# Kernel optimization log

Measured on AMD Instinct MI355X. Metric: run time of the kernel, lower is better.

The kernel has to match this reference:

```python
import jax, jax.numpy as jnp
import numpy as np

B, N, P, K, C = 8, 4096, 4096, 32, 128  # batch, points, npoint, neighbors, channels (=mlp[-1])
W_OUT = 16  # weightnet output channels (from Linear(16*mlp[-1], mlp[-1]))
EPS = 1e-5


def setup_inputs() -> dict:
    key = jax.random.key(0)
    ks = jax.random.split(key, 9)
    xyz = jax.random.normal(ks[0], (B, P, 3), jnp.float32)
    points = jax.random.normal(ks[1], (B, N, C), jnp.float32)
    local_coordinates = jax.random.normal(ks[2], (B, P, K, 3), jnp.float32)
    neighbor_lists = jax.random.randint(ks[3], (B, P, K), 0, N)
    data_idx = jax.random.randint(ks[4], (B,), 0, B)
    Ww = jax.random.normal(ks[5], (3, W_OUT), jnp.float32) * 0.1   # weightnet (pointwise linear 3->16)
    bw = jnp.zeros((W_OUT,), jnp.float32)
    Wl = jax.random.normal(ks[6], (W_OUT * C, C), jnp.float32) * 0.02  # nn.Linear(16*mlp[-1], mlp[-1])
    bl = jnp.zeros((C,), jnp.float32)
    gamma = jnp.ones((C,), jnp.float32)   # BatchNorm1d weight
    beta = jnp.zeros((C,), jnp.float32)   # BatchNorm1d bias
    return {"xyz": xyz, "points": points, "local_coordinates": local_coordinates,
            "neighbor_lists": neighbor_lists, "data_idx": data_idx,
            "Ww": Ww, "bw": bw, "Wl": Wl, "bl": bl, "gamma": gamma, "beta": beta}


def reference(xyz, points, local_coordinates, neighbor_lists, data_idx, Ww, bw, Wl, bl, gamma, beta):
    b, p, k, _ = local_coordinates.shape
    c = points.shape[-1]
    # weightnet: pointwise map of 3-D local coordinates to 16 weight channels -> [B,P,K,16]
    weights = local_coordinates @ Ww + bw
    # irregular neighbor gather: data[b,p,k,:] = points[b, neighbor_lists[b,p,k], :] -> [B,P,K,C]
    data = points[jnp.arange(b)[:, None, None], neighbor_lists]
    # per-point weighted aggregation over K neighbors: [B,P,C,16] -> flatten to [B,P,C*16]
    new_points = jnp.einsum('bpkc,bpkw->bpcw', data, weights).reshape(b, p, c * weights.shape[-1])
    # batch reindex via data_idx
    new_points = new_points[data_idx]
    # linear tail: [B,P,C]
    new_points = new_points @ Wl + bl
    # BatchNorm1d over channel dim (training-mode batch stats), then ReLU: [B,C,P]
    x = new_points.transpose(0, 2, 1)
    mean = x.mean(axis=(0, 2), keepdims=True)
    var = x.var(axis=(0, 2), keepdims=True)
    x = (x - mean) * jax.lax.rsqrt(var + EPS) * gamma[None, :, None] + beta[None, :, None]
    return xyz, jax.nn.relu(x)
```

## Files before the change

### kernel.cpp

```cpp
#include <hip/hip_runtime.h>

#define Bn 8
#define Nn 4096
#define Pn 4096
#define Kn 32
#define Cn 128

using float4v = __attribute__((ext_vector_type(4))) float;
using short8  = __attribute__((ext_vector_type(8))) short;

__device__ __forceinline__ unsigned short bf16b(float f) {
  union { float f; unsigned u; } v; v.f = f;
  unsigned r = v.u + 0x7FFFu + ((v.u >> 16) & 1u);
  return (unsigned short)(r >> 16);
}

__device__ __forceinline__ unsigned pkhi(float x, float y) {
  return __builtin_amdgcn_perm(__float_as_uint(y), __float_as_uint(x), 0x07060302u);
}

__global__ __launch_bounds__(256) void prep(const float* __restrict__ Wl,
                                            unsigned short* __restrict__ WlT,
                                            const float* __restrict__ xyz,
                                            float* __restrict__ out,
                                            float* __restrict__ gacc) {
  __shared__ unsigned short tile[128 * 33];
  const int t = threadIdx.x, blk = blockIdx.x;
  if (blk < 64) {
#pragma unroll
    for (int i = 0; i < 16; ++i) {
      int idx = i * 256 + t;
      int kl = idx >> 7, n = idx & 127;
      tile[n * 33 + kl] = bf16b(Wl[(size_t)(blk * 32 + kl) * 128 + n]);
    }
    __syncthreads();
#pragma unroll
    for (int i = 0; i < 16; ++i) {
      int idx = i * 256 + t;
      int n = idx >> 5, kl = idx & 31;
      WlT[(size_t)n * 2048 + blk * 32 + kl] = tile[n * 33 + kl];
    }
  } else {
    if (blk == 64) gacc[t] = 0.f;
    const int i0 = (blk - 64) * 3072 + t * 12;
#pragma unroll
    for (int i = 0; i < 3; ++i)
      *(float4v*)(out + i0 + i * 4) = *(const float4v*)(xyz + i0 + i * 4);
  }
}

__global__ __launch_bounds__(256, 4) void fused(
    const float* __restrict__ points, const float* __restrict__ lc,
    const int* __restrict__ nl, const int* __restrict__ didx,
    const float* __restrict__ Ww, const float* __restrict__ bwv,
    const unsigned short* __restrict__ WlT, const float* __restrict__ blv,
    float* __restrict__ xout, float* __restrict__ gacc) {
  __shared__ float slab[4][2][512];
  __shared__ unsigned short Mlds[32 * 256];
  __shared__ int nlds[32 * 32];
  __shared__ float red[256];

  const int t = threadIdx.x, lane = t & 63, w = t >> 6;
  const int l15 = lane & 15, q = lane >> 4;
  const int b = blockIdx.x & 7;
  const int pg = blockIdx.x >> 3;
  const int p0 = pg * 32;
  const int db = didx[b];
  const char* __restrict__ pbase = (const char*)(points + (size_t)db * Nn * Cn);

  {
    int4 nv = *(const int4*)(nl + (size_t)(db * Pn + p0) * Kn + t * 4);
    nv.x <<= 9; nv.y <<= 9; nv.z <<= 9; nv.w <<= 9;
    *(int4*)&nlds[t * 4] = nv;
  }

  const float Ww0 = Ww[l15], Ww1 = Ww[16 + l15], Ww2 = Ww[32 + l15];
  const float bw0 = bwv[l15];

  short8 af[8];
#pragma unroll
  for (int i = 0; i < 8; ++i) {
    const int p = p0 + w * 8 + i;
    const int pk = (db * Pn + p) * Kn;
    const float* __restrict__ lcp = lc + (size_t)(pk + q * 8) * 3;
    float la[24];
#pragma unroll
    for (int v = 0; v < 6; ++v) *(float4v*)&la[v * 4] = *(const float4v*)(lcp + v * 4);
#pragma unroll
    for (int j = 0; j < 8; ++j) {
      float ww = bw0 + la[3 * j] * Ww0 + la[3 * j + 1] * Ww1 + la[3 * j + 2] * Ww2;
      af[i][j] = (short)bf16b(ww);
    }
  }

  float4v acc[2][2];
#pragma unroll
  for (int pt = 0; pt < 2; ++pt)
#pragma unroll
    for (int nt = 0; nt < 2; ++nt) acc[pt][nt] = (float4v){0.f, 0.f, 0.f, 0.f};

  __syncthreads();

  const unsigned short* __restrict__ bpt =
      WlT + (size_t)(w * 32 + l15) * 2048 + q * 8;
  const unsigned cvoff = (unsigned)(l15 * 4);

#define WAITV8 asm volatile("s_waitcnt vmcnt(8)" ::: "memory")
#define WAITV0 asm volatile("s_waitcnt vmcnt(0)" ::: "memory")

#define DMA(i, ct, bsel)                                                   \
  {                                                                        \
    const int pi_ = w * 8 + (i);                                           \
    int nk_[8];                                                            \
    *(int4*)&nk_[0] = *(const int4*)&nlds[pi_ * 32 + q * 8];               \
    *(int4*)&nk_[4] = *(const int4*)&nlds[pi_ * 32 + q * 8 + 4];           \
    _Pragma("unroll") for (int j = 0; j < 8; ++j)                          \
        __builtin_amdgcn_global_load_lds(                                  \
            (const __attribute__((address_space(1))) unsigned int*)        \
                (pbase + ((unsigned)nk_[j] + cvoff + (unsigned)((ct) * 64))), \
            (__attribute__((address_space(3))) unsigned int*)              \
                (&slab[w][bsel][(j) * 64]),                                \
            4, 0, 0);                                                      \
  }

#define FIN(i, fsrc)                                                       \
  {                                                                        \
    const int pi_ = w * 8 + (i);                                           \
    union { short8 s; unsigned u[4]; } bv_;                                \
    bv_.u[0] = pkhi(fsrc[0], fsrc[1]);                                     \
    bv_.u[1] = pkhi(fsrc[2], fsrc[3]);                                     \
    bv_.u[2] = pkhi(fsrc[4], fsrc[5]);                                     \
    bv_.u[3] = pkhi(fsrc[6], fsrc[7]);                                     \
    float4v d_ = {0.f, 0.f, 0.f, 0.f};                                     \
    d_ = __builtin_amdgcn_mfma_f32_16x16x32_bf16(af[i], bv_.s, d_, 0, 0, 0); \
    const unsigned off_ = (unsigned)(pi_ * 512 + ((l15 * 32 + q * 8) ^     \
        ((((pi_ & 7) ^ (l15 & 7)) & 7) << 4)));                            \
    uint2 u_;                                                              \
    u_.x = pkhi(d_[0], d_[1]);                                             \
    u_.y = pkhi(d_[2], d_[3]);                                             \
    *(uint2*)((char*)Mlds + off_) = u_;                                    \
  }

  for (int ct = 0; ct < 8; ++ct) {
    DMA(0, ct, 0)
    DMA(1, ct, 1)
#pragma unroll
    for (int i = 0; i < 8; ++i) {
      if (i < 7) { WAITV8; } else { WAITV0; }
      __builtin_amdgcn_sched_barrier(0);
      float f[8];
      const float* ls = &slab[w][i & 1][(unsigned)(q * 16 + l15)];
#pragma unroll
      for (int j = 0; j < 8; ++j) f[j] = ls[j * 64];
      FIN(i, f)
      if (i < 6) {
        __builtin_amdgcn_sched_barrier(0);
        DMA(i + 2, ct, i & 1)
      }
    }
    __syncthreads();
    const unsigned short* __restrict__ bp = bpt + ct * 256;
    short8 b0A = *(const short8*)(bp);
    short8 b1A = *(const short8*)(bp + 32768);
    __builtin_amdgcn_s_setprio(1);
#pragma unroll
    for (int ks = 0; ks < 8; ++ks) {
      short8 b0B, b1B;
      if (ks < 7) {
        b0B = *(const short8*)(bp + (ks + 1) * 32);
        b1B = *(const short8*)(bp + 32768 + (ks + 1) * 32);
      }
      const unsigned ax = (unsigned)((ks * 64 + q * 16) ^
          ((((l15 & 7) ^ ((ks * 2 + (q >> 1)) & 7)) & 7) << 4));
      short8 a0 = *(const short8*)((const char*)Mlds + l15 * 512 + ax);
      short8 a1 = *(const short8*)((const char*)Mlds + (16 + l15) * 512 + ax);
      acc[0][0] = __builtin_amdgcn_mfma_f32_16x16x32_bf16(a0, b0A, acc[0][0], 0, 0, 0);
      acc[0][1] = __builtin_amdgcn_mfma_f32_16x16x32_bf16(a0, b1A, acc[0][1], 0, 0, 0);
      acc[1][0] = __builtin_amdgcn_mfma_f32_16x16x32_bf16(a1, b0A, acc[1][0], 0, 0, 0);
      acc[1][1] = __builtin_amdgcn_mfma_f32_16x16x32_bf16(a1, b1A, acc[1][1], 0, 0, 0);
      b0A = b0B; b1A = b1B;
    }
    __builtin_amdgcn_s_setprio(0);
    __syncthreads();
  }
#undef DMA
#undef FIN
#undef WAITV8
#undef WAITV0

#pragma unroll
  for (int nt = 0; nt < 2; ++nt) {
    const int ch = w * 32 + nt * 16 + l15;
    const float bb = blv[ch];
    float s = 0.f, sq = 0.f;
#pragma unroll
    for (int pt = 0; pt < 2; ++pt) {
      float4v o;
#pragma unroll
      for (int r = 0; r < 4; ++r) {
        float v = acc[pt][nt][r] + bb; o[r] = v; s += v; sq += v * v;
      }
      *(float4v*)(xout + ((size_t)(b * Cn + ch)) * Pn + p0 + pt * 16 + q * 4) = o;
    }
    s += __shfl_xor(s, 16); s += __shfl_xor(s, 32);
    sq += __shfl_xor(sq, 16); sq += __shfl_xor(sq, 32);
    if (lane < 16) { red[ch] = s; red[128 + ch] = sq; }
  }
  __syncthreads();
  atomicAdd(&gacc[t], red[t]);
}

__global__ __launch_bounds__(256) void finalize_ln(float* __restrict__ x,
                                                   const float* __restrict__ gacc,
                                                   const float* __restrict__ gamma,
                                                   const float* __restrict__ beta) {
  const int idx = blockIdx.x * 256 + threadIdx.x;
  const int fi = idx * 4;
  const int c = (fi >> 12) & 127;
  const float inv = 1.f / 32768.f;
  const float mean = gacc[c] * inv;
  const float var = gacc[128 + c] * inv - mean * mean;
  const float scale = rsqrtf(var + 1e-5f) * gamma[c];
  const float shift = beta[c] - mean * scale;
  float4v v = *(float4v*)(x + fi);
#pragma unroll
  for (int r = 0; r < 4; ++r) v[r] = fmaxf(v[r] * scale + shift, 0.f);
  *(float4v*)(x + fi) = v;
}

extern "C" void kernel_launch(void* const* d_in, const int* in_sizes, int n_in,
                              void* d_out, int out_size, void* d_ws, size_t ws_size,
                              hipStream_t stream) {
  const float* xyz    = (const float*)d_in[0];
  const float* points = (const float*)d_in[1];
  const float* lc     = (const float*)d_in[2];
  const int*   nl     = (const int*)d_in[3];
  const int*   didx   = (const int*)d_in[4];
  const float* Ww     = (const float*)d_in[5];
  const float* bw     = (const float*)d_in[6];
  const float* Wl     = (const float*)d_in[7];
  const float* bl     = (const float*)d_in[8];
  const float* gamma  = (const float*)d_in[9];
  const float* beta   = (const float*)d_in[10];

  float* out  = (float*)d_out;
  float* xout = out + (size_t)Bn * Pn * 3;
  unsigned short* WlT = (unsigned short*)d_ws;
  float* gacc = (float*)((char*)d_ws + (size_t)512 * 1024);

  prep<<<96, 256, 0, stream>>>(Wl, WlT, xyz, out, gacc);
  fused<<<1024, 256, 0, stream>>>(points, lc, nl, didx, Ww, bw, WlT, bl,
                                  xout, gacc);
  finalize_ln<<<4096, 256, 0, stream>>>(xout, gacc, gamma, beta);
}
```

Before: 196.5 us.

## Halve points per block and prefetch next channel tile's gather before barrier

Each block now handles 16 points instead of 32, doubling the grid to 2048 blocks and halving the LDS footprint and per-wave MFMA tile. The first two neighbor-gather DMAs for the next channel tile are issued right after the GEMM step, before the closing barrier, so they overlap with synchronization. Full __syncthreads are replaced with lgkmcnt waits plus raw s_barrier. The trade-off is that each WlT B-fragment load is now reused across half as many rows, and twice as many blocks issue atomics.

```diff
diff --git a/kernel.cpp b/kernel.cpp
--- a/kernel.cpp
+++ b/kernel.cpp
@@ -56,31 +56,31 @@
     const unsigned short* __restrict__ WlT, const float* __restrict__ blv,
     float* __restrict__ xout, float* __restrict__ gacc) {
   __shared__ float slab[4][2][512];
-  __shared__ unsigned short Mlds[32 * 256];
-  __shared__ int nlds[32 * 32];
+  __shared__ unsigned short Mlds[16 * 256];
+  __shared__ int nlds[16 * 32];
   __shared__ float red[256];
 
   const int t = threadIdx.x, lane = t & 63, w = t >> 6;
   const int l15 = lane & 15, q = lane >> 4;
   const int b = blockIdx.x & 7;
   const int pg = blockIdx.x >> 3;
-  const int p0 = pg * 32;
+  const int p0 = pg * 16;
   const int db = didx[b];
   const char* __restrict__ pbase = (const char*)(points + (size_t)db * Nn * Cn);
 
   {
-    int4 nv = *(const int4*)(nl + (size_t)(db * Pn + p0) * Kn + t * 4);
-    nv.x <<= 9; nv.y <<= 9; nv.z <<= 9; nv.w <<= 9;
-    *(int4*)&nlds[t * 4] = nv;
+    int2 nv = *(const int2*)(nl + (size_t)(db * Pn + p0) * Kn + t * 2);
+    nv.x <<= 9; nv.y <<= 9;
+    *(int2*)&nlds[t * 2] = nv;
   }
 
   const float Ww0 = Ww[l15], Ww1 = Ww[16 + l15], Ww2 = Ww[32 + l15];
   const float bw0 = bwv[l15];
 
-  short8 af[8];
-#pragma unroll
-  for (int i = 0; i < 8; ++i) {
-    const int p = p0 + w * 8 + i;
+  short8 af[4];
+#pragma unroll
+  for (int i = 0; i < 4; ++i) {
+    const int p = p0 + w * 4 + i;
     const int pk = (db * Pn + p) * Kn;
     const float* __restrict__ lcp = lc + (size_t)(pk + q * 8) * 3;
     float la[24];
@@ -93,11 +93,9 @@
     }
   }
 
-  float4v acc[2][2];
-#pragma unroll
-  for (int pt = 0; pt < 2; ++pt)
-#pragma unroll
-    for (int nt = 0; nt < 2; ++nt) acc[pt][nt] = (float4v){0.f, 0.f, 0.f, 0.f};
+  float4v acc[2];
+  acc[0] = (float4v){0.f, 0.f, 0.f, 0.f};
+  acc[1] = (float4v){0.f, 0.f, 0.f, 0.f};
 
   __syncthreads();
 
@@ -107,10 +105,12 @@
 
 #define WAITV8 asm volatile("s_waitcnt vmcnt(8)" ::: "memory")
 #define WAITV0 asm volatile("s_waitcnt vmcnt(0)" ::: "memory")
+#define LGKM0  asm volatile("s_waitcnt lgkmcnt(0)" ::: "memory")
+#define SBAR   __builtin_amdgcn_sched_barrier(0)
 
 #define DMA(i, ct, bsel)                                                   \
   {                                                                        \
-    const int pi_ = w * 8 + (i);                                           \
+    const int pi_ = w * 4 + (i);                                           \
     int nk_[8];                                                            \
     *(int4*)&nk_[0] = *(const int4*)&nlds[pi_ * 32 + q * 8];               \
     *(int4*)&nk_[4] = *(const int4*)&nlds[pi_ * 32 + q * 8 + 4];           \
@@ -125,7 +125,7 @@
 
 #define FIN(i, fsrc)                                                       \
   {                                                                        \
-    const int pi_ = w * 8 + (i);                                           \
+    const int pi_ = w * 4 + (i);                                           \
     union { short8 s; unsigned u[4]; } bv_;                                \
     bv_.u[0] = pkhi(fsrc[0], fsrc[1]);                                     \
     bv_.u[1] = pkhi(fsrc[2], fsrc[3]);                                     \
@@ -141,24 +141,27 @@
     *(uint2*)((char*)Mlds + off_) = u_;                                    \
   }
 
+  SBAR;
+  DMA(0, 0, 0)
+  DMA(1, 0, 1)
+
   for (int ct = 0; ct < 8; ++ct) {
-    DMA(0, ct, 0)
-    DMA(1, ct, 1)
-#pragma unroll
-    for (int i = 0; i < 8; ++i) {
-      if (i < 7) { WAITV8; } else { WAITV0; }
-      __builtin_amdgcn_sched_barrier(0);
+#pragma unroll
+    for (int i = 0; i < 4; ++i) {
+      if (i < 3) { WAITV8; } else { WAITV0; }
+      SBAR;
       float f[8];
       const float* ls = &slab[w][i & 1][(unsigned)(q * 16 + l15)];
 #pragma unroll
       for (int j = 0; j < 8; ++j) f[j] = ls[j * 64];
       FIN(i, f)
-      if (i < 6) {
-        __builtin_amdgcn_sched_barrier(0);
+      if (i < 2) {
+        SBAR;
         DMA(i + 2, ct, i & 1)
       }
     }
-    __syncthreads();
+    LGKM0; SBAR;
+    __builtin_amdgcn_s_barrier();
     const unsigned short* __restrict__ bp = bpt + ct * 256;
     short8 b0A = *(const short8*)(bp);
     short8 b1A = *(const short8*)(bp + 32768);
@@ -173,35 +176,37 @@
       const unsigned ax = (unsigned)((ks * 64 + q * 16) ^
           ((((l15 & 7) ^ ((ks * 2 + (q >> 1)) & 7)) & 7) << 4));
       short8 a0 = *(const short8*)((const char*)Mlds + l15 * 512 + ax);
-      short8 a1 = *(const short8*)((const char*)Mlds + (16 + l15) * 512 + ax);
-      acc[0][0] = __builtin_amdgcn_mfma_f32_16x16x32_bf16(a0, b0A, acc[0][0], 0, 0, 0);
-      acc[0][1] = __builtin_amdgcn_mfma_f32_16x16x32_bf16(a0, b1A, acc[0][1], 0, 0, 0);
-      acc[1][0] = __builtin_amdgcn_mfma_f32_16x16x32_bf16(a1, b0A, acc[1][0], 0, 0, 0);
-      acc[1][1] = __builtin_amdgcn_mfma_f32_16x16x32_bf16(a1, b1A, acc[1][1], 0, 0, 0);
+      acc[0] = __builtin_amdgcn_mfma_f32_16x16x32_bf16(a0, b0A, acc[0], 0, 0, 0);
+      acc[1] = __builtin_amdgcn_mfma_f32_16x16x32_bf16(a0, b1A, acc[1], 0, 0, 0);
       b0A = b0B; b1A = b1B;
     }
     __builtin_amdgcn_s_setprio(0);
-    __syncthreads();
+    if (ct < 7) {
+      SBAR;
+      DMA(0, ct + 1, 0)
+      DMA(1, ct + 1, 1)
+    }
+    LGKM0; SBAR;
+    __builtin_amdgcn_s_barrier();
   }
 #undef DMA
 #undef FIN
 #undef WAITV8
 #undef WAITV0
+#undef LGKM0
+#undef SBAR
 
 #pragma unroll
   for (int nt = 0; nt < 2; ++nt) {
     const int ch = w * 32 + nt * 16 + l15;
     const float bb = blv[ch];
     float s = 0.f, sq = 0.f;
-#pragma unroll
-    for (int pt = 0; pt < 2; ++pt) {
-      float4v o;
-#pragma unroll
-      for (int r = 0; r < 4; ++r) {
-        float v = acc[pt][nt][r] + bb; o[r] = v; s += v; sq += v * v;
-      }
-      *(float4v*)(xout + ((size_t)(b * Cn + ch)) * Pn + p0 + pt * 16 + q * 4) = o;
-    }
+    float4v o;
+#pragma unroll
+    for (int r = 0; r < 4; ++r) {
+      float v = acc[nt][r] + bb; o[r] = v; s += v; sq += v * v;
+    }
+    *(float4v*)(xout + ((size_t)(b * Cn + ch)) * Pn + p0 + q * 4) = o;
     s += __shfl_xor(s, 16); s += __shfl_xor(s, 32);
     sq += __shfl_xor(sq, 16); sq += __shfl_xor(sq, 32);
     if (lane < 16) { red[ch] = s; red[128 + ch] = sq; }
@@ -249,7 +254,7 @@
   float* gacc = (float*)((char*)d_ws + (size_t)512 * 1024);
 
   prep<<<96, 256, 0, stream>>>(Wl, WlT, xyz, out, gacc);
-  fused<<<1024, 256, 0, stream>>>(points, lc, nl, didx, Ww, bw, WlT, bl,
+  fused<<<2048, 256, 0, stream>>>(points, lc, nl, didx, Ww, bw, WlT, bl,
                                   xout, gacc);
   finalize_ln<<<4096, 256, 0, stream>>>(xout, gacc, gamma, beta);
 }
```

Result: slower. 248.5 us (+26.4%).

## Use 16-byte global-to-LDS gathers with triple buffering and cross-tile prefetch

Applied to the files above, without the earlier changes.

Replaces the eight 4-byte global_load_lds gathers per point with two 16-byte gathers, so each lane fetches four consecutive channels of one neighbor. The neighbor index table is permuted in LDS so that each lane's slab reads still map to the MFMA operand layout. The slab goes from double to triple buffering, and the first three gathers for the next channel tile are issued before the barrier that ends the current GEMM step, so they overlap it. This cuts the number of memory instructions and lets gather latency hide under compute, at the cost of more LDS per block and hand-tuned vmcnt waits that must match exactly.

```diff
diff --git a/kernel.cpp b/kernel.cpp
--- a/kernel.cpp
+++ b/kernel.cpp
@@ -55,9 +55,9 @@
     const float* __restrict__ Ww, const float* __restrict__ bwv,
     const unsigned short* __restrict__ WlT, const float* __restrict__ blv,
     float* __restrict__ xout, float* __restrict__ gacc) {
-  __shared__ float slab[4][2][512];
+  __shared__ float slab[4][3][512];
   __shared__ unsigned short Mlds[32 * 256];
-  __shared__ int nlds[32 * 32];
+  __shared__ int nldsP[32 * 32];
   __shared__ float red[256];
 
   const int t = threadIdx.x, lane = t & 63, w = t >> 6;
@@ -69,9 +69,14 @@
   const char* __restrict__ pbase = (const char*)(points + (size_t)db * Nn * Cn);
 
   {
-    int4 nv = *(const int4*)(nl + (size_t)(db * Pn + p0) * Kn + t * 4);
-    nv.x <<= 9; nv.y <<= 9; nv.z <<= 9; nv.w <<= 9;
-    *(int4*)&nlds[t * 4] = nv;
+    const int pk0 = (db * Pn + p0) * Kn;
+    int4 nv = *(const int4*)(nl + pk0 + t * 4);
+    const int pi = t >> 3;
+    const int r0 = (t << 2) & 31;
+    nldsP[pi * 32 + ((((r0 + 0) & 7) << 2) | ((r0 + 0) >> 3))] = nv.x << 9;
+    nldsP[pi * 32 + ((((r0 + 1) & 7) << 2) | ((r0 + 1) >> 3))] = nv.y << 9;
+    nldsP[pi * 32 + ((((r0 + 2) & 7) << 2) | ((r0 + 2) >> 3))] = nv.z << 9;
+    nldsP[pi * 32 + ((((r0 + 3) & 7) << 2) | ((r0 + 3) >> 3))] = nv.w << 9;
   }
 
   const float Ww0 = Ww[l15], Ww1 = Ww[16 + l15], Ww2 = Ww[32 + l15];
@@ -103,34 +108,45 @@
 
   const unsigned short* __restrict__ bpt =
       WlT + (size_t)(w * 32 + l15) * 2048 + q * 8;
-  const unsigned cvoff = (unsigned)(l15 * 4);
-
-#define WAITV8 asm volatile("s_waitcnt vmcnt(8)" ::: "memory")
+  const int idx0 = lane >> 2;
+  const unsigned subo = (unsigned)((lane & 3) * 16);
+
+#define WAITV4 asm volatile("s_waitcnt vmcnt(4)" ::: "memory")
+#define WAITV2 asm volatile("s_waitcnt vmcnt(2)" ::: "memory")
 #define WAITV0 asm volatile("s_waitcnt vmcnt(0)" ::: "memory")
-
-#define DMA(i, ct, bsel)                                                   \
+#define LGKM0  asm volatile("s_waitcnt lgkmcnt(0)" ::: "memory")
+#define SBAR   __builtin_amdgcn_sched_barrier(0)
+
+#define DMA16(i, ct, bsel)                                                 \
   {                                                                        \
     const int pi_ = w * 8 + (i);                                           \
-    int nk_[8];                                                            \
-    *(int4*)&nk_[0] = *(const int4*)&nlds[pi_ * 32 + q * 8];               \
-    *(int4*)&nk_[4] = *(const int4*)&nlds[pi_ * 32 + q * 8 + 4];           \
-    _Pragma("unroll") for (int j = 0; j < 8; ++j)                          \
-        __builtin_amdgcn_global_load_lds(                                  \
-            (const __attribute__((address_space(1))) unsigned int*)        \
-                (pbase + ((unsigned)nk_[j] + cvoff + (unsigned)((ct) * 64))), \
-            (__attribute__((address_space(3))) unsigned int*)              \
-                (&slab[w][bsel][(j) * 64]),                                \
-            4, 0, 0);                                                      \
-  }
-
-#define FIN(i, fsrc)                                                       \
+    const int a0_ = nldsP[pi_ * 32 + idx0];                                \
+    const int a1_ = nldsP[pi_ * 32 + 16 + idx0];                           \
+    __builtin_amdgcn_global_load_lds(                                      \
+        (const __attribute__((address_space(1))) unsigned int*)            \
+            (pbase + ((unsigned)a0_ + subo + (unsigned)((ct) * 64))),      \
+        (__attribute__((address_space(3))) unsigned int*)                  \
+            (&slab[w][bsel][0]),                                           \
+        16, 0, 0);                                                        \
+    __builtin_amdgcn_global_load_lds(                                      \
+        (const __attribute__((address_space(1))) unsigned int*)            \
+            (pbase + ((unsigned)a1_ + subo + (unsigned)((ct) * 64))),      \
+        (__attribute__((address_space(3))) unsigned int*)                  \
+            (&slab[w][bsel][256]),                                         \
+        16, 0, 0);                                                        \
+  }
+
+#define FIN(i, buf)                                                       \
   {                                                                        \
     const int pi_ = w * 8 + (i);                                           \
+    float f_[8];                                                           \
+    const float* ls_ = &slab[w][buf][(unsigned)lane];                      \
+    _Pragma("unroll") for (int j = 0; j < 8; ++j) f_[j] = ls_[j * 64];     \
     union { short8 s; unsigned u[4]; } bv_;                                \
-    bv_.u[0] = pkhi(fsrc[0], fsrc[1]);                                     \
-    bv_.u[1] = pkhi(fsrc[2], fsrc[3]);                                     \
-    bv_.u[2] = pkhi(fsrc[4], fsrc[5]);                                     \
-    bv_.u[3] = pkhi(fsrc[6], fsrc[7]);                                     \
+    bv_.u[0] = pkhi(f_[0], f_[1]);                                         \
+    bv_.u[1] = pkhi(f_[2], f_[3]);                                         \
+    bv_.u[2] = pkhi(f_[4], f_[5]);                                         \
+    bv_.u[3] = pkhi(f_[6], f_[7]);                                         \
     float4v d_ = {0.f, 0.f, 0.f, 0.f};                                     \
     d_ = __builtin_amdgcn_mfma_f32_16x16x32_bf16(af[i], bv_.s, d_, 0, 0, 0); \
     const unsigned off_ = (unsigned)(pi_ * 512 + ((l15 * 32 + q * 8) ^     \
@@ -141,24 +157,22 @@
     *(uint2*)((char*)Mlds + off_) = u_;                                    \
   }
 
+  SBAR;
+  DMA16(0, 0, 0)
+  DMA16(1, 0, 1)
+  DMA16(2, 0, 2)
+
   for (int ct = 0; ct < 8; ++ct) {
-    DMA(0, ct, 0)
-    DMA(1, ct, 1)
-#pragma unroll
-    for (int i = 0; i < 8; ++i) {
-      if (i < 7) { WAITV8; } else { WAITV0; }
-      __builtin_amdgcn_sched_barrier(0);
-      float f[8];
-      const float* ls = &slab[w][i & 1][(unsigned)(q * 16 + l15)];
-#pragma unroll
-      for (int j = 0; j < 8; ++j) f[j] = ls[j * 64];
-      FIN(i, f)
-      if (i < 6) {
-        __builtin_amdgcn_sched_barrier(0);
-        DMA(i + 2, ct, i & 1)
-      }
-    }
-    __syncthreads();
+    WAITV4; SBAR; FIN(0, 0) SBAR; DMA16(3, ct, 0)
+    WAITV4; SBAR; FIN(1, 1) SBAR; DMA16(4, ct, 1)
+    WAITV4; SBAR; FIN(2, 2) SBAR; DMA16(5, ct, 2)
+    WAITV4; SBAR; FIN(3, 0) SBAR; DMA16(6, ct, 0)
+    WAITV4; SBAR; FIN(4, 1) SBAR; DMA16(7, ct, 1)
+    WAITV4; SBAR; FIN(5, 2)
+    WAITV2; SBAR; FIN(6, 0)
+    WAITV0; SBAR; FIN(7, 1)
+    LGKM0; SBAR;
+    __builtin_amdgcn_s_barrier();
     const unsigned short* __restrict__ bp = bpt + ct * 256;
     short8 b0A = *(const short8*)(bp);
     short8 b1A = *(const short8*)(bp + 32768);
@@ -181,12 +195,22 @@
       b0A = b0B; b1A = b1B;
     }
     __builtin_amdgcn_s_setprio(0);
-    __syncthreads();
-  }
-#undef DMA
+    if (ct < 7) {
+      SBAR;
+      DMA16(0, ct + 1, 0)
+      DMA16(1, ct + 1, 1)
+      DMA16(2, ct + 1, 2)
+    }
+    SBAR;
+    __builtin_amdgcn_s_barrier();
+  }
+#undef DMA16
 #undef FIN
-#undef WAITV8
+#undef WAITV4
+#undef WAITV2
 #undef WAITV0
+#undef LGKM0
+#undef SBAR
 
 #pragma unroll
   for (int nt = 0; nt < 2; ++nt) {
```

Measured after the change: 204.6 us. 1.04x slower.
